# Optimization experiments

Measured on AMD Instinct MI355X. Metric: run time of the kernel, lower is better.

The kernel has to match this reference:

```python
import jax, jax.numpy as jnp
import numpy as np

C = 16            # NCA_channels
LCD = 3           # living_channel_dim
ALPHA = 0.1       # alpha_living_threshold


def _alive(x):
    # F.max_pool3d(x[:, LCD], k=3, s=1, p=1) -> shape [B, D, H, W]
    a = x[:, LCD]
    return jax.lax.reduce_window(a, -jnp.inf, jax.lax.max,
                                 (1, 3, 3, 3), (1, 1, 1, 1), 'SAME')


def _thresh(alive):
    th = ALPHA * jnp.max(alive)
    return jnp.where(jnp.isnan(th), -jnp.inf, th)


def _pw(h, w, b):
    # 1x1x1 Conv3d == per-voxel matmul. h: [B,c,D,H,W], w: [o,c]
    return jnp.einsum('bcdhw,oc->bodhw', h, w) + b[None, :, None, None, None]


def _update(x, w_perc, b_perc, w1, b1, w2, b2, w3, b3):
    alive0 = _alive(x)
    pre_mask = alive0 > _thresh(alive0)
    # depthwise perception conv: C -> 3C, groups=C, k=3, pad=1
    out = jax.lax.conv_general_dilated(
        x, w_perc, (1, 1, 1), 'SAME',
        dimension_numbers=('NCDHW', 'OIDHW', 'NCDHW'),
        feature_group_count=C) + b_perc[None, :, None, None, None]
    # per-voxel MLP: 3C -> h -> h -> C (tanh on hidden layers only)
    out = jnp.tanh(_pw(out, w1, b1))
    out = jnp.tanh(_pw(out, w2, b2))
    out = _pw(out, w3, b3)
    # normalise=False, replace=False -> residual add
    x = x + out
    alive1 = _alive(x)
    post_mask = alive1 > _thresh(alive1)
    life = pre_mask & post_mask          # [B, D, H, W]
    # torch x * life_mask (broadcast valid for B=1)
    return x * life[:, None].astype(x.dtype)


def setup_inputs() -> dict:
    key = jax.random.key(0)
    ks = jax.random.split(key, 10)
    D = 96
    x = jax.random.normal(ks[0], (1, C, D, D, D), dtype=jnp.float32)
    s = 0.1  # keep tanh-NCA dynamics stable
    return {
        'x': x,
        'w_perc': jax.random.normal(ks[1], (3 * C, 1, 3, 3, 3), jnp.float32) * s,
        'b_perc': jax.random.normal(ks[2], (3 * C,), jnp.float32) * s,
        'w1': jax.random.normal(ks[3], (64, 3 * C), jnp.float32) * s,
        'b1': jax.random.normal(ks[4], (64,), jnp.float32) * s,
        'w2': jax.random.normal(ks[5], (64, 64), jnp.float32) * s,
        'b2': jax.random.normal(ks[6], (64,), jnp.float32) * s,
        'w3': jax.random.normal(ks[7], (C, 64), jnp.float32) * s,
        'b3': jax.random.normal(ks[8], (C,), jnp.float32) * s,
        'steps': 4,
        'reading_channel': 4,
        'policy_layers': 2,
        'inOut_out': 48,
    }


def reference(x, w_perc, b_perc, w1, b1, w2, b2, w3, b3,
              steps, reading_channel, policy_layers, inOut_out):
    del reading_channel, policy_layers  # only used for visualization/PCA paths
    for _ in range(steps):
        x = _update(x, w_perc, b_perc, w1, b1, w2, b2, w3, b3)
        # x[:, :, -1, inOutdim[1]:, :] = 0.0
        x = x.at[:, :, -1, inOut_out:, :].set(0.0)
    return x
```

## Files before the change

kernel.cpp:

```cpp
#include <hip/hip_runtime.h>

#define Cn 16
#define Dn 96
#define Sn (Dn*Dn*Dn)
#define DSTRIDE (Dn*Dn)
#define ENC_NEG_INF 0x007FFFFFu
#define HROW 68

typedef float v2f __attribute__((ext_vector_type(2)));
typedef float v4f __attribute__((ext_vector_type(4)));
typedef _Float16 v4h __attribute__((ext_vector_type(4)));

__device__ __forceinline__ v2f ld2(const float* p){
    v2f r; __builtin_memcpy(&r, p, 8); return r;
}
__device__ __forceinline__ unsigned encf(float f){
    unsigned u = __float_as_uint(f);
    return (u & 0x80000000u) ? ~u : (u | 0x80000000u);
}
__device__ __forceinline__ float decf(unsigned u){
    return (u & 0x80000000u) ? __uint_as_float(u ^ 0x80000000u) : __uint_as_float(~u);
}
__device__ __forceinline__ float ftanh(float x){
    float t = __expf(2.0f*x);
    return 1.0f - __fdividef(2.0f, t + 1.0f);
}
__device__ __forceinline__ int clampi(int v){ return v<0?0:(v>Dn-1?Dn-1:v); }

__global__ void init_kernel(unsigned* __restrict__ maxv){
    if (threadIdx.x < 16) maxv[threadIdx.x] = ENC_NEG_INF;
}

__global__ void tr_kernel(const float* __restrict__ wp, const float* __restrict__ bp,
                          float* __restrict__ wpT, float* __restrict__ bpP){
    const int i = blockIdx.x*256 + threadIdx.x;
    if (i < 1296){ const int t=i/48, r=i%48, q=r>>4, c=r&15; wpT[i] = wp[(3*c+q)*27 + t]; }
    if (i < 48)  { const int q=i>>4, c=i&15; bpP[i] = bp[3*c + q]; }
}

__global__ void pack_kernel(const float* __restrict__ w1, const float* __restrict__ w2,
                            const float* __restrict__ w3,
                            _Float16* __restrict__ w1Fh, _Float16* __restrict__ w1Fl,
                            _Float16* __restrict__ w2Fh, _Float16* __restrict__ w2Fl,
                            _Float16* __restrict__ w3Fh, _Float16* __restrict__ w3Fl){
    const int i = blockIdx.x*256 + threadIdx.x;
    if (i < 3072){
        const int e = i & 3, l = (i>>2) & 63, t = i >> 8;
        const int ks = t % 3, nt = t / 3;
        const int k = ks*16 + ((l>>4)<<2) + e;
        const int n = nt*16 + (l & 15);
        const int c = k & 15, q = k >> 4;
        const float v = w1[n*48 + 3*c + q];
        const _Float16 hh = (_Float16)v;
        w1Fh[i] = hh; w1Fl[i] = (_Float16)(v - (float)hh);
    }
    if (i < 4096){
        const int e = i & 3, l = (i>>2) & 63, t = i >> 8;
        const int ks = t & 3, nt = t >> 2;
        const int k = ks*16 + ((l>>4)<<2) + e;
        const int n = nt*16 + (l & 15);
        const float v = w2[n*64 + k];
        const _Float16 hh = (_Float16)v;
        w2Fh[i] = hh; w2Fl[i] = (_Float16)(v - (float)hh);
    }
    if (i < 1024){
        const int e = i & 3, l = (i>>2) & 63, ks = i >> 8;
        const int k = ks*16 + ((l>>4)<<2) + e;
        const int n = l & 15;
        const float v = w3[n*64 + k];
        const _Float16 hh = (_Float16)v;
        w3Fh[i] = hh; w3Fl[i] = (_Float16)(v - (float)hh);
    }
}

__global__ __launch_bounds__(256) void prep_kernel(const float* __restrict__ x3,
    float* __restrict__ maskA, unsigned* __restrict__ slot)
{
    const int idx = blockIdx.x*256 + threadIdx.x;
    maskA[idx] = 1.0f;
    float v = x3[idx];
    #pragma unroll
    for (int o=32;o;o>>=1) v = fmaxf(v, __shfl_down(v, o));
    __shared__ float red[4];
    const int lane = threadIdx.x & 63, wid = threadIdx.x >> 6;
    if (lane==0) red[wid]=v;
    __syncthreads();
    if (threadIdx.x==0){
        float m = fmaxf(fmaxf(red[0],red[1]), fmaxf(red[2],red[3]));
        atomicMax(slot, encf(m));
    }
}

struct XBuf { float x[16]; float m; int v; };

__device__ __forceinline__ void prefetch_t(int t, int d, int h, int w,
    const float* __restrict__ xin, const float* __restrict__ min_, XBuf& B)
{
    const int zz = d + t/9 - 1;
    const int yy = h + (t/3)%3 - 1;
    const int xx = w + t%3 - 1;
    const int zc = clampi(zz), yc = clampi(yy), xc = clampi(xx);
    B.v = (zz==zc) & (yy==yc) & (xx==xc);
    const int noff = zc*DSTRIDE + yc*Dn + xc;
    B.m = min_[noff];
    #pragma unroll
    for (int c=0;c<16;++c) B.x[c] = xin[(size_t)c*Sn + noff];
}

__device__ __forceinline__ void accum_t(int t, const XBuf& A,
    const float* __restrict__ wpT, v2f* pv)
{
    const float mv = A.v ? A.m : 0.0f;
    const v2f mvv = {mv, mv};
    const float* wrow = wpT + t*48;
    #pragma unroll
    for (int i=0;i<8;++i){
        v2f xv = {A.x[2*i], A.x[2*i+1]};
        v2f xm = xv * mvv;
        pv[i]    = __builtin_elementwise_fma(ld2(wrow + 2*i),      xm, pv[i]);
        pv[8+i]  = __builtin_elementwise_fma(ld2(wrow + 16 + 2*i), xm, pv[8+i]);
        pv[16+i] = __builtin_elementwise_fma(ld2(wrow + 32 + 2*i), xm, pv[16+i]);
    }
}

__global__ __launch_bounds__(256, 2) void update_kernel(
    const float* __restrict__ xin, const float* __restrict__ min_,
    float* __restrict__ xout,
    const float* __restrict__ wpT, const float* __restrict__ bpP,
    const _Float16* __restrict__ w1Fh, const _Float16* __restrict__ w1Fl,
    const float* __restrict__ b1,
    const _Float16* __restrict__ w2Fh, const _Float16* __restrict__ w2Fl,
    const float* __restrict__ b2,
    const _Float16* __restrict__ w3Fh, const _Float16* __restrict__ w3Fl,
    const float* __restrict__ b3,
    unsigned* __restrict__ slot_post)
{
    __shared__ __align__(16) char smemRaw[2*256*HROW*2];
    _Float16* sHi = (_Float16*)smemRaw;
    _Float16* sLo = (_Float16*)(smemRaw + 256*HROW*2);
    float*    sO  = (float*)smemRaw;

    const int tid = threadIdx.x;
    const int w = blockIdx.x*32 + (tid & 31);
    const int h = blockIdx.y*8  + (tid >> 5);
    const int d = blockIdx.z;
    const int idx = d*DSTRIDE + h*Dn + w;

    const int lane = tid & 63;
    const int wv   = tid >> 6;
    const int lr   = lane & 15;
    const int lg   = lane >> 4;

    v2f pv[24];
    #pragma unroll
    for (int j=0;j<24;++j) pv[j] = ld2(bpP + 2*j);

    XBuf A, B;
    prefetch_t(0, d, h, w, xin, min_, A);
    #pragma unroll 1
    for (int t=0; t<26; t+=2){
        prefetch_t(t+1, d, h, w, xin, min_, B);
        accum_t(t, A, wpT, pv);
        prefetch_t(t+2, d, h, w, xin, min_, A);
        accum_t(t+1, B, wpT, pv);
    }
    accum_t(26, A, wpT, pv);

    {
        _Float16* pa = sHi + tid*HROW;
        _Float16* pb = sLo + tid*HROW;
        #pragma unroll
        for (int j=0;j<12;++j){
            const float f0=pv[2*j].x, f1=pv[2*j].y, f2=pv[2*j+1].x, f3=pv[2*j+1].y;
            v4h hi = {(_Float16)f0,(_Float16)f1,(_Float16)f2,(_Float16)f3};
            v4h lo = {(_Float16)(f0-(float)hi[0]), (_Float16)(f1-(float)hi[1]),
                      (_Float16)(f2-(float)hi[2]), (_Float16)(f3-(float)hi[3])};
            *(v4h*)(pa + 4*j) = hi;
            *(v4h*)(pb + 4*j) = lo;
        }
    }

    const int arow = 64*wv + lr;

    v4f acc1[4][4];
    #pragma unroll
    for (int nt=0;nt<4;++nt){
        const float bv = b1[nt*16 + lr];
        #pragma unroll
        for (int mt=0;mt<4;++mt) acc1[mt][nt] = (v4f){bv,bv,bv,bv};
    }
    #pragma unroll
    for (int ks=0;ks<3;++ks){
        v4h bh[4], bl[4];
        #pragma unroll
        for (int nt=0;nt<4;++nt){
            bh[nt] = *(const v4h*)(w1Fh + (((nt*3+ks)*64 + lane) << 2));
            bl[nt] = *(const v4h*)(w1Fl + (((nt*3+ks)*64 + lane) << 2));
        }
        #pragma unroll
        for (int mt=0;mt<4;++mt){
            const int ro = (arow + 16*mt)*HROW + ks*16 + lg*4;
            const v4h ah = *(const v4h*)(sHi + ro);
            const v4h al = *(const v4h*)(sLo + ro);
            #pragma unroll
            for (int nt=0;nt<4;++nt){
                acc1[mt][nt] = __builtin_amdgcn_mfma_f32_16x16x16f16(ah, bh[nt], acc1[mt][nt], 0,0,0);
                acc1[mt][nt] = __builtin_amdgcn_mfma_f32_16x16x16f16(al, bh[nt], acc1[mt][nt], 0,0,0);
                acc1[mt][nt] = __builtin_amdgcn_mfma_f32_16x16x16f16(ah, bl[nt], acc1[mt][nt], 0,0,0);
            }
        }
    }
    #pragma unroll
    for (int mt=0;mt<4;++mt){
        const int rbase = 64*wv + 16*mt + lg*4;
        #pragma unroll
        for (int nt=0;nt<4;++nt){
            #pragma unroll
            for (int r=0;r<4;++r){
                const float v = ftanh(acc1[mt][nt][r]);
                const _Float16 hh = (_Float16)v;
                sHi[(rbase + r)*HROW + nt*16 + lr] = hh;
                sLo[(rbase + r)*HROW + nt*16 + lr] = (_Float16)(v - (float)hh);
            }
        }
    }

    v4f acc2[4][4];
    #pragma unroll
    for (int nt=0;nt<4;++nt){
        const float bv = b2[nt*16 + lr];
        #pragma unroll
        for (int mt=0;mt<4;++mt) acc2[mt][nt] = (v4f){bv,bv,bv,bv};
    }
    #pragma unroll
    for (int ks=0;ks<4;++ks){
        v4h bh[4], bl[4];
        #pragma unroll
        for (int nt=0;nt<4;++nt){
            bh[nt] = *(const v4h*)(w2Fh + (((nt*4+ks)*64 + lane) << 2));
            bl[nt] = *(const v4h*)(w2Fl + (((nt*4+ks)*64 + lane) << 2));
        }
        #pragma unroll
        for (int mt=0;mt<4;++mt){
            const int ro = (arow + 16*mt)*HROW + ks*16 + lg*4;
            const v4h ah = *(const v4h*)(sHi + ro);
            const v4h al = *(const v4h*)(sLo + ro);
            #pragma unroll
            for (int nt=0;nt<4;++nt){
                acc2[mt][nt] = __builtin_amdgcn_mfma_f32_16x16x16f16(ah, bh[nt], acc2[mt][nt], 0,0,0);
                acc2[mt][nt] = __builtin_amdgcn_mfma_f32_16x16x16f16(al, bh[nt], acc2[mt][nt], 0,0,0);
                acc2[mt][nt] = __builtin_amdgcn_mfma_f32_16x16x16f16(ah, bl[nt], acc2[mt][nt], 0,0,0);
            }
        }
    }
    #pragma unroll
    for (int mt=0;mt<4;++mt){
        const int rbase = 64*wv + 16*mt + lg*4;
        #pragma unroll
        for (int nt=0;nt<4;++nt){
            #pragma unroll
            for (int r=0;r<4;++r){
                const float v = ftanh(acc2[mt][nt][r]);
                const _Float16 hh = (_Float16)v;
                sHi[(rbase + r)*HROW + nt*16 + lr] = hh;
                sLo[(rbase + r)*HROW + nt*16 + lr] = (_Float16)(v - (float)hh);
            }
        }
    }

    v4f acc3[4];
    {
        const float bv = b3[lr];
        #pragma unroll
        for (int mt=0;mt<4;++mt) acc3[mt] = (v4f){bv,bv,bv,bv};
    }
    #pragma unroll
    for (int ks=0;ks<4;++ks){
        const v4h bh = *(const v4h*)(w3Fh + ((ks*64 + lane) << 2));
        const v4h bl = *(const v4h*)(w3Fl + ((ks*64 + lane) << 2));
        #pragma unroll
        for (int mt=0;mt<4;++mt){
            const int ro = (arow + 16*mt)*HROW + ks*16 + lg*4;
            const v4h ah = *(const v4h*)(sHi + ro);
            const v4h al = *(const v4h*)(sLo + ro);
            acc3[mt] = __builtin_amdgcn_mfma_f32_16x16x16f16(ah, bh, acc3[mt], 0,0,0);
            acc3[mt] = __builtin_amdgcn_mfma_f32_16x16x16f16(al, bh, acc3[mt], 0,0,0);
            acc3[mt] = __builtin_amdgcn_mfma_f32_16x16x16f16(ah, bl, acc3[mt], 0,0,0);
        }
    }
    #pragma unroll
    for (int mt=0;mt<4;++mt){
        const int rbase = 64*wv + 16*mt + lg*4;
        #pragma unroll
        for (int r=0;r<4;++r)
            sO[(rbase + r)*(HROW/2) + lr] = acc3[mt][r];
    }

    const float mcen = min_[idx];
    const float* orow = sO + tid*(HROW/2);
    float v3 = 0.0f;
    #pragma unroll
    for (int c=0;c<16;++c){
        const float xn = fmaf(xin[(size_t)c*Sn+idx], mcen, orow[c]);
        xout[(size_t)c*Sn+idx] = xn;
        if (c==3) v3 = xn;
    }

    #pragma unroll
    for (int o=32;o;o>>=1) v3 = fmaxf(v3, __shfl_down(v3, o));
    if ((tid & 63) == 0) atomicMax(slot_post, encf(v3));
}

__global__ __launch_bounds__(256) void mask_kernel(
    const float* __restrict__ xin3, const float* __restrict__ min_,
    const float* __restrict__ xout3, float* __restrict__ mout,
    const unsigned* __restrict__ slot_pre, const unsigned* __restrict__ slot_post,
    unsigned* __restrict__ slot_next)
{
    const int idx = blockIdx.x*256 + threadIdx.x;
    const int w = idx % Dn;
    const int h = (idx / Dn) % Dn;
    const int d = idx / DSTRIDE;
    const float th0 = 0.1f * decf(*slot_pre);
    const float th1 = 0.1f * decf(*slot_post);
    float a0 = -INFINITY, a1 = -INFINITY;
    #pragma unroll
    for (int t=0;t<27;++t){
        const int dz=t/9-1, dy=(t/3)%3-1, dx=t%3-1;
        const int zz=d+dz, yy=h+dy, xx=w+dx;
        if ((unsigned)zz<(unsigned)Dn && (unsigned)yy<(unsigned)Dn &&
            (unsigned)xx<(unsigned)Dn){
            const int noff = idx + dz*DSTRIDE + dy*Dn + dx;
            a0 = fmaxf(a0, xin3[noff]*min_[noff]);
            a1 = fmaxf(a1, xout3[noff]);
        }
    }
    const bool life = (a0 > th0) && (a1 > th1) && !(d==Dn-1 && h>=48);
    const float mv = life ? 1.0f : 0.0f;
    mout[idx] = mv;

    float f3 = xout3[idx]*mv;
    #pragma unroll
    for (int o=32;o;o>>=1) f3 = fmaxf(f3, __shfl_down(f3, o));
    __shared__ float red[4];
    const int lane = threadIdx.x & 63, wid = threadIdx.x >> 6;
    if (lane==0) red[wid]=f3;
    __syncthreads();
    if (threadIdx.x==0){
        float m = fmaxf(fmaxf(red[0],red[1]), fmaxf(red[2],red[3]));
        atomicMax(slot_next, encf(m));
    }
}

__global__ __launch_bounds__(256) void apply_kernel(float* __restrict__ x,
    const float* __restrict__ mk)
{
    const int idx = blockIdx.x*256 + threadIdx.x;
    const float m = mk[idx];
    #pragma unroll
    for (int c=0;c<Cn;++c) x[(size_t)c*Sn+idx] *= m;
}

extern "C" void kernel_launch(void* const* d_in, const int* in_sizes, int n_in,
                              void* d_out, int out_size, void* d_ws, size_t ws_size,
                              hipStream_t stream)
{
    const float* x0 = (const float*)d_in[0];
    const float* wp = (const float*)d_in[1];
    const float* bp = (const float*)d_in[2];
    const float* w1 = (const float*)d_in[3];
    const float* b1 = (const float*)d_in[4];
    const float* w2 = (const float*)d_in[5];
    const float* b2 = (const float*)d_in[6];
    const float* w3 = (const float*)d_in[7];
    const float* b3 = (const float*)d_in[8];
    float* out = (float*)d_out;

    float* xbuf  = (float*)d_ws;
    float* maskA = xbuf + (size_t)Cn*Sn;
    float* maskB = maskA + Sn;
    unsigned* maxv = (unsigned*)(maskB + Sn);
    float* wpT = (float*)(maxv + 16);
    float* bpP = wpT + 1296;
    _Float16* w1Fh = (_Float16*)(bpP + 48);
    _Float16* w1Fl = w1Fh + 3072;
    _Float16* w2Fh = w1Fl + 3072;
    _Float16* w2Fl = w2Fh + 4096;
    _Float16* w3Fh = w2Fl + 4096;
    _Float16* w3Fl = w3Fh + 1024;

    init_kernel<<<1, 64, 0, stream>>>(maxv);
    tr_kernel<<<6, 256, 0, stream>>>(wp, bp, wpT, bpP);
    pack_kernel<<<16, 256, 0, stream>>>(w1, w2, w3, w1Fh, w1Fl, w2Fh, w2Fl, w3Fh, w3Fl);
    prep_kernel<<<Sn/256, 256, 0, stream>>>(x0 + (size_t)3*Sn, maskA, &maxv[0]);

    const float* xi[4] = {x0,   xbuf, out,  xbuf};
    float*       xo[4] = {xbuf, out,  xbuf, out};
    const float* mi[4] = {maskA, maskB, maskA, maskB};
    float*       mo[4] = {maskB, maskA, maskB, maskA};

    dim3 ugrid(Dn/32, Dn/8, Dn);
    for (int s=0; s<4; ++s){
        update_kernel<<<ugrid, 256, 0, stream>>>(xi[s], mi[s], xo[s],
            wpT, bpP, w1Fh, w1Fl, b1, w2Fh, w2Fl, b2, w3Fh, w3Fl, b3, &maxv[2*s+1]);
        mask_kernel<<<Sn/256, 256, 0, stream>>>(xi[s]+(size_t)3*Sn, mi[s],
            xo[s]+(size_t)3*Sn, mo[s], &maxv[2*s], &maxv[2*s+1], &maxv[2*s+2]);
    }
    apply_kernel<<<Sn/256, 256, 0, stream>>>(out, maskA);
}
```

Measured before the change: 1.307 ms.

## Switch intermediate state to channel-last layout for vectorized neighbor loads

Adds a transpose kernel that converts the input to a voxel-major, channel-last layout. Update steps then read all 16 channels of each stencil neighbor as four 16-byte vector loads instead of 16 strided scalar loads, and write intermediates in the same layout. The final step writes back channel-first, and the mask kernel reads channel 3 at stride 16. The shared-memory row pitch also changes from 68 to 70, presumably to reduce bank conflicts. Costs: an extra transpose pass, and the mask kernel's strided channel-3 reads lose coalescing.

```diff
diff --git a/kernel.cpp b/kernel.cpp
--- a/kernel.cpp
+++ b/kernel.cpp
@@ -5,7 +5,7 @@
 #define Sn (Dn*Dn*Dn)
 #define DSTRIDE (Dn*Dn)
 #define ENC_NEG_INF 0x007FFFFFu
-#define HROW 68
+#define HROW 70
 
 typedef float v2f __attribute__((ext_vector_type(2)));
 typedef float v4f __attribute__((ext_vector_type(4)));
@@ -91,10 +91,25 @@
     }
 }
 
-struct XBuf { float x[16]; float m; int v; };
+__global__ __launch_bounds__(256) void transpose_kernel(const float* __restrict__ x,
+    float* __restrict__ xT)
+{
+    const int idx = blockIdx.x*256 + threadIdx.x;
+    float v[16];
+    #pragma unroll
+    for (int c=0;c<16;++c) v[c] = x[(size_t)c*Sn + idx];
+    float* dst = xT + (size_t)idx*16;
+    #pragma unroll
+    for (int k=0;k<4;++k){
+        v4f t = {v[4*k], v[4*k+1], v[4*k+2], v[4*k+3]};
+        __builtin_memcpy(dst + 4*k, &t, 16);
+    }
+}
+
+struct XBufT { v4f x[4]; float m; int v; };
 
 __device__ __forceinline__ void prefetch_t(int t, int d, int h, int w,
-    const float* __restrict__ xin, const float* __restrict__ min_, XBuf& B)
+    const float* __restrict__ xT, const float* __restrict__ min_, XBufT& B)
 {
     const int zz = d + t/9 - 1;
     const int yy = h + (t/3)%3 - 1;
@@ -103,11 +118,12 @@
     B.v = (zz==zc) & (yy==yc) & (xx==xc);
     const int noff = zc*DSTRIDE + yc*Dn + xc;
     B.m = min_[noff];
-    #pragma unroll
-    for (int c=0;c<16;++c) B.x[c] = xin[(size_t)c*Sn + noff];
-}
-
-__device__ __forceinline__ void accum_t(int t, const XBuf& A,
+    const float* p = xT + (size_t)noff*16;
+    #pragma unroll
+    for (int k=0;k<4;++k) __builtin_memcpy(&B.x[k], p + 4*k, 16);
+}
+
+__device__ __forceinline__ void accum_t(int t, const XBufT& A,
     const float* __restrict__ wpT, v2f* pv)
 {
     const float mv = A.v ? A.m : 0.0f;
@@ -115,7 +131,7 @@
     const float* wrow = wpT + t*48;
     #pragma unroll
     for (int i=0;i<8;++i){
-        v2f xv = {A.x[2*i], A.x[2*i+1]};
+        v2f xv = { A.x[i>>1][(i&1)*2], A.x[i>>1][(i&1)*2+1] };
         v2f xm = xv * mvv;
         pv[i]    = __builtin_elementwise_fma(ld2(wrow + 2*i),      xm, pv[i]);
         pv[8+i]  = __builtin_elementwise_fma(ld2(wrow + 16 + 2*i), xm, pv[8+i]);
@@ -124,8 +140,8 @@
 }
 
 __global__ __launch_bounds__(256, 2) void update_kernel(
-    const float* __restrict__ xin, const float* __restrict__ min_,
-    float* __restrict__ xout,
+    const float* __restrict__ xinT, const float* __restrict__ min_,
+    float* __restrict__ xout, const int final_,
     const float* __restrict__ wpT, const float* __restrict__ bpP,
     const _Float16* __restrict__ w1Fh, const _Float16* __restrict__ w1Fl,
     const float* __restrict__ b1,
@@ -155,13 +171,13 @@
     #pragma unroll
     for (int j=0;j<24;++j) pv[j] = ld2(bpP + 2*j);
 
-    XBuf A, B;
-    prefetch_t(0, d, h, w, xin, min_, A);
+    XBufT A, B;
+    prefetch_t(0, d, h, w, xinT, min_, A);
     #pragma unroll 1
     for (int t=0; t<26; t+=2){
-        prefetch_t(t+1, d, h, w, xin, min_, B);
+        prefetch_t(t+1, d, h, w, xinT, min_, B);
         accum_t(t, A, wpT, pv);
-        prefetch_t(t+2, d, h, w, xin, min_, A);
+        prefetch_t(t+2, d, h, w, xinT, min_, A);
         accum_t(t+1, B, wpT, pv);
     }
     accum_t(26, A, wpT, pv);
@@ -297,13 +313,27 @@
     }
 
     const float mcen = min_[idx];
+    const float* xrow = xinT + (size_t)idx*16;
     const float* orow = sO + tid*(HROW/2);
     float v3 = 0.0f;
-    #pragma unroll
-    for (int c=0;c<16;++c){
-        const float xn = fmaf(xin[(size_t)c*Sn+idx], mcen, orow[c]);
-        xout[(size_t)c*Sn+idx] = xn;
-        if (c==3) v3 = xn;
+    if (!final_){
+        float* dst = xout + (size_t)idx*16;
+        #pragma unroll
+        for (int k=0;k<4;++k){
+            v4f xc; __builtin_memcpy(&xc, xrow + 4*k, 16);
+            v4f on;
+            #pragma unroll
+            for (int j=0;j<4;++j) on[j] = fmaf(xc[j], mcen, orow[4*k+j]);
+            __builtin_memcpy(dst + 4*k, &on, 16);
+            if (k==0) v3 = on[3];
+        }
+    } else {
+        #pragma unroll
+        for (int c=0;c<16;++c){
+            const float xn = fmaf(xrow[c], mcen, orow[c]);
+            xout[(size_t)c*Sn+idx] = xn;
+            if (c==3) v3 = xn;
+        }
     }
 
     #pragma unroll
@@ -312,8 +342,8 @@
 }
 
 __global__ __launch_bounds__(256) void mask_kernel(
-    const float* __restrict__ xin3, const float* __restrict__ min_,
-    const float* __restrict__ xout3, float* __restrict__ mout,
+    const float* __restrict__ xinT, const float* __restrict__ min_,
+    const float* __restrict__ xo3, const int out_t, float* __restrict__ mout,
     const unsigned* __restrict__ slot_pre, const unsigned* __restrict__ slot_post,
     unsigned* __restrict__ slot_next)
 {
@@ -331,15 +361,16 @@
         if ((unsigned)zz<(unsigned)Dn && (unsigned)yy<(unsigned)Dn &&
             (unsigned)xx<(unsigned)Dn){
             const int noff = idx + dz*DSTRIDE + dy*Dn + dx;
-            a0 = fmaxf(a0, xin3[noff]*min_[noff]);
-            a1 = fmaxf(a1, xout3[noff]);
+            a0 = fmaxf(a0, xinT[(size_t)noff*16+3]*min_[noff]);
+            a1 = fmaxf(a1, out_t ? xo3[(size_t)noff*16+3] : xo3[noff]);
         }
     }
     const bool life = (a0 > th0) && (a1 > th1) && !(d==Dn-1 && h>=48);
     const float mv = life ? 1.0f : 0.0f;
     mout[idx] = mv;
 
-    float f3 = xout3[idx]*mv;
+    const float xv3 = out_t ? xo3[(size_t)idx*16+3] : xo3[idx];
+    float f3 = xv3*mv;
     #pragma unroll
     for (int o=32;o;o>>=1) f3 = fmaxf(f3, __shfl_down(f3, o));
     __shared__ float red[4];
@@ -376,8 +407,8 @@
     const float* b3 = (const float*)d_in[8];
     float* out = (float*)d_out;
 
-    float* xbuf  = (float*)d_ws;
-    float* maskA = xbuf + (size_t)Cn*Sn;
+    float* T0    = (float*)d_ws;
+    float* maskA = T0 + (size_t)Cn*Sn;
     float* maskB = maskA + Sn;
     unsigned* maxv = (unsigned*)(maskB + Sn);
     float* wpT = (float*)(maxv + 16);
@@ -388,23 +419,28 @@
     _Float16* w2Fl = w2Fh + 4096;
     _Float16* w3Fh = w2Fl + 4096;
     _Float16* w3Fl = w3Fh + 1024;
+    float* T1 = out;
 
     init_kernel<<<1, 64, 0, stream>>>(maxv);
     tr_kernel<<<6, 256, 0, stream>>>(wp, bp, wpT, bpP);
     pack_kernel<<<16, 256, 0, stream>>>(w1, w2, w3, w1Fh, w1Fl, w2Fh, w2Fl, w3Fh, w3Fl);
     prep_kernel<<<Sn/256, 256, 0, stream>>>(x0 + (size_t)3*Sn, maskA, &maxv[0]);
-
-    const float* xi[4] = {x0,   xbuf, out,  xbuf};
-    float*       xo[4] = {xbuf, out,  xbuf, out};
-    const float* mi[4] = {maskA, maskB, maskA, maskB};
-    float*       mo[4] = {maskB, maskA, maskB, maskA};
+    transpose_kernel<<<Sn/256, 256, 0, stream>>>(x0, T1);
+
+    const float* xiT[4] = {T1, T0, T1, T0};
+    float*       xo[4]  = {T0, T1, T0, out};
+    const int    fin[4] = {0, 0, 0, 1};
+    const float* mx3[4] = {T0, T1, T0, out + (size_t)3*Sn};
+    const int    mot[4] = {1, 1, 1, 0};
+    const float* mi[4]  = {maskA, maskB, maskA, maskB};
+    float*       mo[4]  = {maskB, maskA, maskB, maskA};
 
     dim3 ugrid(Dn/32, Dn/8, Dn);
     for (int s=0; s<4; ++s){
-        update_kernel<<<ugrid, 256, 0, stream>>>(xi[s], mi[s], xo[s],
+        update_kernel<<<ugrid, 256, 0, stream>>>(xiT[s], mi[s], xo[s], fin[s],
             wpT, bpP, w1Fh, w1Fl, b1, w2Fh, w2Fl, b2, w3Fh, w3Fl, b3, &maxv[2*s+1]);
-        mask_kernel<<<Sn/256, 256, 0, stream>>>(xi[s]+(size_t)3*Sn, mi[s],
-            xo[s]+(size_t)3*Sn, mo[s], &maxv[2*s], &maxv[2*s+1], &maxv[2*s+2]);
+        mask_kernel<<<Sn/256, 256, 0, stream>>>(xiT[s], mi[s],
+            mx3[s], mot[s], mo[s], &maxv[2*s], &maxv[2*s+1], &maxv[2*s+2]);
     }
     apply_kernel<<<Sn/256, 256, 0, stream>>>(out, maskA);
 }
```

New measurement: 1.964 ms. +50.2%, slower.
